# Kernel tuning notes

Hardware: AMD Instinct MI355X
Metric: run time of the kernel (lower is better)

The kernel has to match this reference:

```python
import jax, jax.numpy as jnp
import numpy as np

B = 128
IN_FEATURES = 1024
HIDDEN = 512
N_OPS = 2        # operators = [T_Norm.min, T_Conorm.max]
N_EDGE_TYPES = 2 # [no_edge, normal_edge]
NO_EDGE_OFFSET_T_NORM = 1.0
NO_EDGE_OFFSET_T_CONORM = 0.0


def setup_inputs() -> dict:
    key = jax.random.key(0)
    x = jax.random.uniform(key, (B, IN_FEATURES), dtype=jnp.float32)
    sizes = [IN_FEATURES, HIDDEN, IN_FEATURES]
    inp = {"x": x}
    for li in range(len(sizes) - 1):
        fi, fo = sizes[li], sizes[li + 1]
        # counts are initialized to ones in the torch module (buffers, not trained by grad)
        inp[f"etc{li}"] = jnp.ones((fo, N_OPS, fi, N_EDGE_TYPES), dtype=jnp.float32)
        inp[f"otc{li}"] = jnp.ones((fo, N_OPS), dtype=jnp.float32)
    return inp


def _layer_forward(key, x, edge_type_count, operator_type_count):
    # x: [B, in]; edge_type_count: [out, n_ops, in, n_et]; operator_type_count: [out, n_ops]
    k_op, k_edge = jax.random.split(key)
    # hard gumbel-softmax == argmax over (logits + gumbel noise), tau irrelevant for argmax
    g_op = jax.random.gumbel(k_op, operator_type_count.shape, dtype=jnp.float32)
    op_idx = jnp.argmax(operator_type_count + g_op, axis=-1)          # [out], 0=min(T_Norm), 1=max(T_Conorm)
    g_e = jax.random.gumbel(k_edge, edge_type_count.shape, dtype=jnp.float32)
    sel_idx = jnp.argmax(edge_type_count + g_e, axis=-1)              # [out, n_ops, in]
    sel = jax.nn.one_hot(sel_idx, N_EDGE_TYPES, dtype=x.dtype)        # [out, n_ops, in, n_et]
    # edge_selection = op_edge_selection[range(out), op_indices]
    out_f = sel.shape[0]
    edge_sel = sel[jnp.arange(out_f), op_idx]                         # [out, in, n_et]
    # edge_type_values: no_edge -> 0 (+1 offset if operator is T_Norm/min), normal_edge -> x
    no_edge_val = jnp.where(op_idx == 0, NO_EDGE_OFFSET_T_NORM, NO_EDGE_OFFSET_T_CONORM)  # [out]
    a = edge_sel[..., 0] * no_edge_val[:, None]                       # [out, in]
    b = edge_sel[None, :, :, 1] * x[:, None, :]                       # [B, out, in]
    edge_values = jnp.maximum(a[None, :, :], b)                       # max over edge-type dim (one-hot -> 2 terms)
    out_min = jnp.min(edge_values, axis=-1)                           # [B, out]
    out_max = jnp.max(edge_values, axis=-1)                           # [B, out]
    return jnp.where(op_idx[None, :] == 0, out_min, out_max)


def reference(x, etc0, otc0, etc1, otc1):
    base = jax.random.key(42)
    h = _layer_forward(jax.random.fold_in(base, 0), x, etc0, otc0)
    out = _layer_forward(jax.random.fold_in(base, 1), h, etc1, otc1)
    return out
```

## Files before the change

kernel.cpp:

```cpp
#include <hip/hip_runtime.h>
#include <stdint.h>


__host__ __device__ inline uint32_t rotl32(uint32_t x, uint32_t d) {
  return (x << d) | (x >> (32u - d));
}

__host__ __device__ inline void threefry2x32(uint32_t k0, uint32_t k1,
                                             uint32_t x0, uint32_t x1,
                                             uint32_t* o0, uint32_t* o1) {
  uint32_t ks0 = k0, ks1 = k1, ks2 = k0 ^ k1 ^ 0x1BD11BDAu;
  x0 += ks0; x1 += ks1;
#define TF_R(r) { x0 += x1; x1 = rotl32(x1, r); x1 ^= x0; }
  TF_R(13u) TF_R(15u) TF_R(26u) TF_R(6u)
  x0 += ks1; x1 += ks2 + 1u;
  TF_R(17u) TF_R(29u) TF_R(16u) TF_R(24u)
  x0 += ks2; x1 += ks0 + 2u;
  TF_R(13u) TF_R(15u) TF_R(26u) TF_R(6u)
  x0 += ks0; x1 += ks1 + 3u;
  TF_R(17u) TF_R(29u) TF_R(16u) TF_R(24u)
  x0 += ks1; x1 += ks2 + 4u;
  TF_R(13u) TF_R(15u) TF_R(26u) TF_R(6u)
  x0 += ks2; x1 += ks0 + 5u;
#undef TF_R
  *o0 = x0; *o1 = x1;
}

__device__ __forceinline__ uint32_t rbits32(uint32_t k0, uint32_t k1,
                                            uint32_t e) {
  uint32_t a, b;
  threefry2x32(k0, k1, 0u, e, &a, &b);
  return a ^ b;
}

__device__ __forceinline__ double flog(double x) {
  long long bits = __double_as_longlong(x);
  int e = (int)(bits >> 52) - 1023;
  double m = __longlong_as_double((bits & 0x000fffffffffffffLL) |
                                  0x3ff0000000000000LL);
  if (m > 1.4142135623730951) { m *= 0.5; e += 1; }
  double mp1 = m + 1.0;
  double r = __builtin_amdgcn_rcp(mp1);
  r = r * __builtin_fma(-mp1, r, 2.0);
  r = r * __builtin_fma(-mp1, r, 2.0);
  double z = (m - 1.0) * r;
  double w = z * z;
  double p = 1.0 / 15.0;
  p = __builtin_fma(p, w, 1.0 / 13.0);
  p = __builtin_fma(p, w, 1.0 / 11.0);
  p = __builtin_fma(p, w, 1.0 / 9.0);
  p = __builtin_fma(p, w, 1.0 / 7.0);
  p = __builtin_fma(p, w, 1.0 / 5.0);
  p = __builtin_fma(p, w, 1.0 / 3.0);
  p = __builtin_fma(p, w, 1.0);
  double de = (double)e;
  const double ln2_hi = 6.93147180369123816490e-01;
  const double ln2_lo = 1.90821492927058770002e-10;
  return __builtin_fma(de, ln2_hi,
                       __builtin_fma(2.0 * z, p, de * ln2_lo));
}

__device__ __forceinline__ float gumbel_from_u32(uint32_t bits) {
  uint32_t fb = (bits >> 9) | 0x3f800000u;
  float f = __uint_as_float(fb) - 1.0f;
  float u = (f > 0.0f) ? f : 1.17549435e-38f;
  float l1 = (float)flog((double)u);
  float l2 = (float)flog((double)(-l1));
  return -l2;
}

__device__ __forceinline__ float fast_ln(float x) {
  uint32_t b = __float_as_uint(x);
  int e = (int)(b >> 23) - 127;
  float m = __uint_as_float((b & 0x007fffffu) | 0x3f800000u);
  if (m > 1.41421356f) { m *= 0.5f; e += 1; }
  float z = (m - 1.0f) * __builtin_amdgcn_rcpf(m + 1.0f);
  float w = z * z;
  float p = __builtin_fmaf(w, __builtin_fmaf(w, 0.14285715f, 0.2f),
                           0.33333334f);
  float q = __builtin_fmaf(w, p, 1.0f);
  float lnm = 2.0f * z * q;
  return __builtin_fmaf((float)e, 0.69314718f, lnm);
}

__device__ __forceinline__ float gumbel_fast(uint32_t bits) {
  uint32_t fb = (bits >> 9) | 0x3f800000u;
  float f = __uint_as_float(fb) - 1.0f;
  float u = (f > 0.0f) ? f : 1.17549435e-38f;
  float l1 = fast_ln(u);
  return -fast_ln(-l1);
}

__device__ __forceinline__ float guard_tau(float a, float b) {
  return 1e-3f + 3.1e-5f * (fabsf(a) + fabsf(b));
}

__global__ __launch_bounds__(256) void edges_kernel(
    const float* __restrict__ etcA, const float* __restrict__ otcA,
    uint32_t oa0, uint32_t oa1, uint32_t ea0, uint32_t ea1,
    int* __restrict__ opA, unsigned long long* __restrict__ selA,
    const float* __restrict__ etcB, const float* __restrict__ otcB,
    uint32_t ob0, uint32_t ob1, uint32_t eb0, uint32_t eb1,
    int* __restrict__ opB, unsigned long long* __restrict__ selB) {
  int gid = blockIdx.x * 256 + threadIdx.x;
  const float *etc, *otc; unsigned long long* selw; int* opx;
  uint32_t ok0, ok1, k0, k1; int inlog;
  if (gid < 512 * 1024) {
    etc = etcA; otc = otcA; opx = opA; selw = selA;
    ok0 = oa0; ok1 = oa1; k0 = ea0; k1 = ea1; inlog = 10;
  } else {
    gid -= 512 * 1024;
    etc = etcB; otc = otcB; opx = opB; selw = selB;
    ok0 = ob0; ok1 = ob1; k0 = eb0; k1 = eb1; inlog = 9;
  }
  int o = gid >> inlog;
  int lane = threadIdx.x & 63;

  float vf = 0.0f;
  if (lane < 2)
    vf = otc[2 * o + lane] +
         gumbel_fast(rbits32(ok0, ok1, (uint32_t)(2 * o + lane)));
  float v0 = __shfl(vf, 0, 64);
  float v1 = __shfl(vf, 1, 64);
  float dop = v1 - v0;
  int j;
  if (__builtin_expect(fabsf(dop) <= guard_tau(v0, v1), 0)) {
    float ve0 = otc[2 * o] +
                gumbel_from_u32(rbits32(ok0, ok1, (uint32_t)(2 * o)));
    float ve1 = otc[2 * o + 1] +
                gumbel_from_u32(rbits32(ok0, ok1, (uint32_t)(2 * o + 1)));
    j = (ve1 > ve0) ? 1 : 0;
  } else {
    j = (dop > 0.0f) ? 1 : 0;
  }
  if (threadIdx.x == 0) opx[o] = j;

  int i = gid & ((1 << inlog) - 1);
  uint32_t e0 = (uint32_t)((((o * 2 + j) << inlog) + i) * 2);
  uint32_t r0 = rbits32(k0, k1, e0);
  uint32_t r1 = rbits32(k0, k1, e0 + 1u);
  const float* c = etc + (size_t)e0;
  float c0 = c[0], c1 = c[1];
  float t0 = c0 + gumbel_fast(r0);
  float t1 = c1 + gumbel_fast(r1);
  float diff = t1 - t0;
  bool sel;
  if (__builtin_expect(fabsf(diff) <= guard_tau(t0, t1), 0)) {
    sel = (c1 + gumbel_from_u32(r1)) > (c0 + gumbel_from_u32(r0));
  } else {
    sel = diff > 0.0f;
  }
  unsigned long long m = __ballot(sel ? 1 : 0);
  if (lane == 0) selw[gid >> 6] = m;
}

template <int IN_F, int OUT_F>
__global__ __launch_bounds__(256) void forward_kernel(
    const float* __restrict__ x, const int* __restrict__ opidx,
    const unsigned long long* __restrict__ selw, float* __restrict__ out) {
  constexpr int W32 = IN_F / 32;
  constexpr int CH = IN_F / 256;
  const uint32_t* __restrict__ sel32 = (const uint32_t*)selw;
  int wave = blockIdx.x * 4 + (threadIdx.x >> 6);
  int lane = threadIdx.x & 63;
  int og = wave % (OUT_F / 8);
  int b  = wave / (OUT_F / 8);
  int o0 = og * 8;
  int sh = (lane * 4) & 31;
  int wb = lane >> 3;

  float sgn[8], neu[8];
  int opv[8];
#pragma unroll
  for (int jj = 0; jj < 8; ++jj) {
    int op = opidx[o0 + jj];
    opv[jj] = op;
    sgn[jj] = op ? 1.0f : -1.0f;
    neu[jj] = op ? 0.0f : -1.0f;
  }
  float acc[8];
#pragma unroll
  for (int jj = 0; jj < 8; ++jj) acc[jj] = -1e30f;
  const float* xrow = x + (size_t)b * IN_F;
#pragma unroll
  for (int cc = 0; cc < CH; ++cc) {
    int i0 = cc * 256 + lane * 4;
    float4 xv = *(const float4*)(xrow + i0);
    int w32 = cc * 8 + wb;
#pragma unroll
    for (int jj = 0; jj < 8; ++jj) {
      uint32_t m32 = sel32[(o0 + jj) * W32 + w32];
      uint32_t b4 = (m32 >> sh) & 0xFu;
      float s = sgn[jj], n = neu[jj];
      float v0 = (b4 & 1u) ? s * xv.x : n;
      float v1 = (b4 & 2u) ? s * xv.y : n;
      float v2 = (b4 & 4u) ? s * xv.z : n;
      float v3 = (b4 & 8u) ? s * xv.w : n;
      acc[jj] = fmaxf(acc[jj], fmaxf(fmaxf(v0, v1), fmaxf(v2, v3)));
    }
  }
#pragma unroll
  for (int d = 1; d < 64; d <<= 1) {
#pragma unroll
    for (int jj = 0; jj < 8; ++jj)
      acc[jj] = fmaxf(acc[jj], __shfl_xor(acc[jj], d, 64));
  }
  if (lane == 0) {
    float4 r0, r1;
    r0.x = opv[0] ? acc[0] : -acc[0];
    r0.y = opv[1] ? acc[1] : -acc[1];
    r0.z = opv[2] ? acc[2] : -acc[2];
    r0.w = opv[3] ? acc[3] : -acc[3];
    r1.x = opv[4] ? acc[4] : -acc[4];
    r1.y = opv[5] ? acc[5] : -acc[5];
    r1.z = opv[6] ? acc[6] : -acc[6];
    r1.w = opv[7] ? acc[7] : -acc[7];
    float* op = out + (size_t)b * OUT_F + o0;
    *(float4*)op = r0;
    *(float4*)(op + 4) = r1;
  }
}

extern "C" void kernel_launch(void* const* d_in, const int* in_sizes, int n_in,
                              void* d_out, int out_size, void* d_ws, size_t ws_size,
                              hipStream_t stream) {
  const float* x    = (const float*)d_in[0];
  const float* etc0 = (const float*)d_in[1];
  const float* otc0 = (const float*)d_in[2];
  const float* etc1 = (const float*)d_in[3];
  const float* otc1 = (const float*)d_in[4];
  float* out = (float*)d_out;

  uint32_t K0a, K0b, K1a, K1b;
  threefry2x32(0u, 42u, 0u, 0u, &K0a, &K0b);
  threefry2x32(0u, 42u, 0u, 1u, &K1a, &K1b);
  uint32_t op0k0, op0k1, ed0k0, ed0k1;
  threefry2x32(K0a, K0b, 0u, 0u, &op0k0, &op0k1);
  threefry2x32(K0a, K0b, 0u, 1u, &ed0k0, &ed0k1);
  uint32_t op1k0, op1k1, ed1k0, ed1k1;
  threefry2x32(K1a, K1b, 0u, 0u, &op1k0, &op1k1);
  threefry2x32(K1a, K1b, 0u, 1u, &ed1k0, &ed1k1);

  char* wsb = (char*)d_ws;
  int* opidx0 = (int*)wsb;
  int* opidx1 = (int*)(wsb + 2048);
  unsigned long long* selw0 = (unsigned long long*)(wsb + 8192);
  unsigned long long* selw1 = (unsigned long long*)(wsb + 8192 + 65536);
  float* h = (float*)(wsb + 8192 + 131072);

  hipLaunchKernelGGL(edges_kernel, dim3(4096), dim3(256), 0, stream,
                     etc0, otc0, op0k0, op0k1, ed0k0, ed0k1, opidx0, selw0,
                     etc1, otc1, op1k0, op1k1, ed1k0, ed1k1, opidx1, selw1);
  hipLaunchKernelGGL((forward_kernel<1024, 512>), dim3(2048), dim3(256), 0,
                     stream, x, opidx0, selw0, h);
  hipLaunchKernelGGL((forward_kernel<512, 1024>), dim3(4096), dim3(256), 0,
                     stream, h, opidx1, selw1, out);
}
```

Baseline: 104.3 us.

## Skip Gumbel transcendental math via integer bit-gap comparison and batch edges per thread

```diff
diff --git a/kernel.cpp b/kernel.cpp
--- a/kernel.cpp
+++ b/kernel.cpp
@@ -95,6 +95,32 @@
   return 1e-3f + 3.1e-5f * (fabsf(a) + fabsf(b));
 }
 
+__device__ __noinline__ bool sel_exact(float c0, float c1,
+                                       uint32_t r0, uint32_t r1) {
+  return (c1 + gumbel_from_u32(r1)) > (c0 + gumbel_from_u32(r0));
+}
+
+__device__ __forceinline__ bool sel_guarded(float c0, float c1,
+                                            uint32_t r0, uint32_t r1) {
+  float t0 = c0 + gumbel_fast(r0);
+  float t1 = c1 + gumbel_fast(r1);
+  float diff = t1 - t0;
+  if (__builtin_expect(fabsf(diff) <= guard_tau(t0, t1), 0))
+    return sel_exact(c0, c1, r0, r1);
+  return diff > 0.0f;
+}
+
+__device__ __forceinline__ bool sel_cmp(float c0, float c1,
+                                        uint32_t r0, uint32_t r1) {
+  if (__builtin_expect(c0 == c1, 1)) {
+    int gap = (int)(r1 >> 9) - (int)(r0 >> 9);
+    int T = 8 + (int)((fabsf(c0) + 16.0f) * 3.0f);
+    if (__builtin_expect(gap >= T || gap <= -T, 1)) return gap > 0;
+    return sel_guarded(c0, c1, r0, r1);
+  }
+  return sel_guarded(c0, c1, r0, r1);
+}
+
 __global__ __launch_bounds__(256) void edges_kernel(
     const float* __restrict__ etcA, const float* __restrict__ otcA,
     uint32_t oa0, uint32_t oa1, uint32_t ea0, uint32_t ea1,
@@ -102,56 +128,58 @@
     const float* __restrict__ etcB, const float* __restrict__ otcB,
     uint32_t ob0, uint32_t ob1, uint32_t eb0, uint32_t eb1,
     int* __restrict__ opB, unsigned long long* __restrict__ selB) {
-  int gid = blockIdx.x * 256 + threadIdx.x;
+  int widx = threadIdx.x >> 6;
+  int lane = threadIdx.x & 63;
   const float *etc, *otc; unsigned long long* selw; int* opx;
-  uint32_t ok0, ok1, k0, k1; int inlog;
-  if (gid < 512 * 1024) {
+  uint32_t ok0, ok1, k0, k1;
+  int inlog, o, ibase, wordbase;
+  bool store_op;
+  if (blockIdx.x < 512) {
     etc = etcA; otc = otcA; opx = opA; selw = selA;
     ok0 = oa0; ok1 = oa1; k0 = ea0; k1 = ea1; inlog = 10;
+    o = blockIdx.x;
+    ibase = widx * 256;
+    wordbase = o * 16 + widx * 4;
+    store_op = (threadIdx.x == 0);
   } else {
-    gid -= 512 * 1024;
     etc = etcB; otc = otcB; opx = opB; selw = selB;
     ok0 = ob0; ok1 = ob1; k0 = eb0; k1 = eb1; inlog = 9;
-  }
-  int o = gid >> inlog;
-  int lane = threadIdx.x & 63;
-
-  float vf = 0.0f;
-  if (lane < 2)
-    vf = otc[2 * o + lane] +
-         gumbel_fast(rbits32(ok0, ok1, (uint32_t)(2 * o + lane)));
-  float v0 = __shfl(vf, 0, 64);
-  float v1 = __shfl(vf, 1, 64);
-  float dop = v1 - v0;
-  int j;
-  if (__builtin_expect(fabsf(dop) <= guard_tau(v0, v1), 0)) {
-    float ve0 = otc[2 * o] +
-                gumbel_from_u32(rbits32(ok0, ok1, (uint32_t)(2 * o)));
-    float ve1 = otc[2 * o + 1] +
-                gumbel_from_u32(rbits32(ok0, ok1, (uint32_t)(2 * o + 1)));
-    j = (ve1 > ve0) ? 1 : 0;
-  } else {
-    j = (dop > 0.0f) ? 1 : 0;
-  }
-  if (threadIdx.x == 0) opx[o] = j;
-
-  int i = gid & ((1 << inlog) - 1);
-  uint32_t e0 = (uint32_t)((((o * 2 + j) << inlog) + i) * 2);
-  uint32_t r0 = rbits32(k0, k1, e0);
-  uint32_t r1 = rbits32(k0, k1, e0 + 1u);
-  const float* c = etc + (size_t)e0;
-  float c0 = c[0], c1 = c[1];
-  float t0 = c0 + gumbel_fast(r0);
-  float t1 = c1 + gumbel_fast(r1);
-  float diff = t1 - t0;
-  bool sel;
-  if (__builtin_expect(fabsf(diff) <= guard_tau(t0, t1), 0)) {
-    sel = (c1 + gumbel_from_u32(r1)) > (c0 + gumbel_from_u32(r0));
-  } else {
-    sel = diff > 0.0f;
-  }
-  unsigned long long m = __ballot(sel ? 1 : 0);
-  if (lane == 0) selw[gid >> 6] = m;
+    int bb = blockIdx.x - 512;
+    o = bb * 2 + (widx >> 1);
+    ibase = (widx & 1) * 256;
+    wordbase = o * 8 + (widx & 1) * 4;
+    store_op = ((widx & 1) == 0) && (lane == 0);
+  }
+
+  uint32_t rop = 0; float cop = 0.0f;
+  if (lane < 2) {
+    rop = rbits32(ok0, ok1, (uint32_t)(2 * o + lane));
+    cop = otc[2 * o + lane];
+  }
+  uint32_t rop0 = (uint32_t)__shfl((int)rop, 0, 64);
+  uint32_t rop1 = (uint32_t)__shfl((int)rop, 1, 64);
+  float cop0 = __shfl(cop, 0, 64);
+  float cop1 = __shfl(cop, 1, 64);
+  int j = sel_cmp(cop0, cop1, rop0, rop1) ? 1 : 0;
+  if (store_op) opx[o] = j;
+
+  uint32_t ebase = (uint32_t)((o * 2 + j) << (inlog + 1));
+  const float* cbase = etc + (size_t)ebase;
+  bool selv[4];
+#pragma unroll
+  for (int p = 0; p < 4; ++p) {
+    int i = ibase + p * 64 + lane;
+    uint32_t e0 = ebase + (uint32_t)(2 * i);
+    uint32_t r0 = rbits32(k0, k1, e0);
+    uint32_t r1 = rbits32(k0, k1, e0 + 1u);
+    float2 cc = *(const float2*)(cbase + 2 * i);
+    selv[p] = sel_cmp(cc.x, cc.y, r0, r1);
+  }
+#pragma unroll
+  for (int p = 0; p < 4; ++p) {
+    unsigned long long m = __ballot(selv[p] ? 1 : 0);
+    if (lane == 0) selw[wordbase + p] = m;
+  }
 }
 
 template <int IN_F, int OUT_F>
@@ -248,7 +276,7 @@
   unsigned long long* selw1 = (unsigned long long*)(wsb + 8192 + 65536);
   float* h = (float*)(wsb + 8192 + 131072);
 
-  hipLaunchKernelGGL(edges_kernel, dim3(4096), dim3(256), 0, stream,
+  hipLaunchKernelGGL(edges_kernel, dim3(1024), dim3(256), 0, stream,
                      etc0, otc0, op0k0, op0k1, ed0k0, ed0k1, opidx0, selw0,
                      etc1, otc1, op1k0, op1k1, ed1k0, ed1k1, opidx1, selw1);
   hipLaunchKernelGGL((forward_kernel<1024, 512>), dim3(2048), dim3(256), 0,
```

After: 100.1 us (median of 2 runs). -4.0%, faster.
